# Optimization experiments

Hardware: AMD Instinct MI355X
Metric: run time of the kernel (lower is better)

Reference implementation:

```python
import jax, jax.numpy as jnp
import numpy as np

V = 20000
E = 40000
NODE_IN = 74
EDGE_IN = 12
D = 64            # node_out_feats
EH = 128          # edge_hidden_feats
STEPS = 6         # num_step_message_passing


def setup_inputs() -> dict:
    key = jax.random.key(0)
    ks = jax.random.split(key, 16)
    s = lambda k, shape, scale=0.05: jax.random.normal(k, shape, dtype=jnp.float32) * scale
    return {
        "node_feats": jax.random.normal(ks[0], (V, NODE_IN), dtype=jnp.float32),
        "edge_feats": jax.random.normal(ks[1], (E, EDGE_IN), dtype=jnp.float32),
        "src": jax.random.randint(ks[2], (E,), 0, V),
        "dst": jax.random.randint(ks[3], (E,), 0, V),
        # project_node_feats: Linear(NODE_IN, D) + ReLU
        "proj_W": s(ks[4], (D, NODE_IN)),
        "proj_b": jnp.zeros((D,), jnp.float32),
        # NNConv edge network: Linear(EDGE_IN, EH) -> ReLU -> Linear(EH, D*D)
        "en_W1": s(ks[5], (EH, EDGE_IN)),
        "en_b1": jnp.zeros((EH,), jnp.float32),
        "en_W2": s(ks[6], (D * D, EH)),
        "en_b2": jnp.zeros((D * D,), jnp.float32),
        # NNConv output bias
        "conv_b": jnp.zeros((D,), jnp.float32),
        # single-layer GRU (PyTorch gate order r, z, n)
        "gru_Wih": s(ks[7], (3 * D, D)),
        "gru_Whh": s(ks[8], (3 * D, D)),
        "gru_bih": jnp.zeros((3 * D,), jnp.float32),
        "gru_bhh": jnp.zeros((3 * D,), jnp.float32),
        # MLPPredictor: Linear(2*D, 1)
        "pred_W": s(ks[9], (1, 2 * D)),
        "pred_b": jnp.zeros((1,), jnp.float32),
    }


def reference(node_feats, edge_feats, src, dst, proj_W, proj_b,
              en_W1, en_b1, en_W2, en_b2, conv_b,
              gru_Wih, gru_Whh, gru_bih, gru_bhh, pred_W, pred_b):
    nV = node_feats.shape[0]
    # project node features
    h = jax.nn.relu(node_feats @ proj_W.T + proj_b)  # (V, D)
    # per-edge weight matrices from the edge network (constant across steps)
    ew = jax.nn.relu(edge_feats @ en_W1.T + en_b1) @ en_W2.T + en_b2  # (E, D*D)
    ew = ew.reshape(-1, D, D)  # (E, D, D)

    def step(h, _):
        # NNConv (aggregator='sum'): m_e = h[src_e] @ W_e, sum at dst, + bias
        m = jnp.einsum('ei,eio->eo', h[src], ew)               # (E, D)
        neigh = jax.ops.segment_sum(m, dst, num_segments=nV)   # (V, D)
        x = jax.nn.relu(neigh + conv_b)
        # GRU update; hidden == h (they coincide in the original loop)
        gi = x @ gru_Wih.T + gru_bih
        gh = h @ gru_Whh.T + gru_bhh
        i_r, i_z, i_n = jnp.split(gi, 3, axis=-1)
        h_r, h_z, h_n = jnp.split(gh, 3, axis=-1)
        r = jax.nn.sigmoid(i_r + h_r)
        z = jax.nn.sigmoid(i_z + h_z)
        n = jnp.tanh(i_n + r * h_n)
        h_new = (1.0 - z) * n + z * h
        return h_new, None

    h, _ = jax.lax.scan(step, h, None, length=STEPS)
    # MLPPredictor: per-edge gather-concat-linear
    score = jnp.concatenate([h[src], h[dst]], axis=1) @ pred_W.T + pred_b  # (E, 1)
    return score
```

## Files before the change

kernel.cpp:

```cpp
#include <hip/hip_runtime.h>
#include <hip/hip_bf16.h>
#include <cstdint>

#define NV 20000
#define NE 40000
#define NODE_IN 74
#define EDGE_IN 12
#define D 64
#define EHID 128
#define NSTEPS 6

typedef __bf16 bf16x8 __attribute__((ext_vector_type(8)));
typedef float f32x4 __attribute__((ext_vector_type(4)));

__global__ __launch_bounds__(256) void k_prep(
    const float* __restrict__ nf, const float* __restrict__ pjW, const float* __restrict__ pjb,
    float* __restrict__ h, float* __restrict__ neigh,
    const float* __restrict__ ef, const float* __restrict__ W1, const float* __restrict__ b1,
    __hip_bfloat16* __restrict__ t_bf,
    const float* __restrict__ W2, __hip_bfloat16* __restrict__ w2b,
    const float* __restrict__ b2, __hip_bfloat16* __restrict__ b2t,
    const float* __restrict__ Wih, const float* __restrict__ Whh,
    __hip_bfloat16* __restrict__ Bhi, __hip_bfloat16* __restrict__ Blo) {
  __shared__ float smem[4 * NODE_IN];
  int tid = threadIdx.x;
  int bx = blockIdx.x;
  if (bx < 5000) {
    int nb = bx * 4;
    for (int idx = tid; idx < 4 * NODE_IN; idx += 256)
      smem[idx] = nf[(size_t)nb * NODE_IN + idx];
    __syncthreads();
    int nl = tid >> 6, o = tid & 63;
    float acc = pjb[o];
#pragma unroll
    for (int i = 0; i < NODE_IN; ++i) acc = fmaf(smem[nl * NODE_IN + i], pjW[o * NODE_IN + i], acc);
    h[(size_t)(nb + nl) * D + o] = fmaxf(acc, 0.f);
    neigh[(size_t)(nb + nl) * D + o] = 0.f;
  } else if (bx < 25000) {
    int eb = (bx - 5000) * 2;
    if (tid < 2 * EDGE_IN)
      smem[tid] = ef[(size_t)eb * EDGE_IN + tid];
    __syncthreads();
    int el = tid >> 7, k = tid & 127;
    float acc = b1[k];
#pragma unroll
    for (int j = 0; j < EDGE_IN; ++j) acc = fmaf(smem[el * EDGE_IN + j], W1[k * EDGE_IN + j], acc);
    t_bf[(size_t)(eb + el) * EHID + k] = __float2bfloat16(fmaxf(acc, 0.f));
  } else if (bx < 27048) {
    int idx = (bx - 25000) * 256 + tid;
    w2b[idx] = __float2bfloat16(W2[idx]);
  } else if (bx < 27064) {
    int idx = (bx - 27048) * 256 + tid;
    int o = idx >> 6, i = idx & 63;
    b2t[o * 64 + i] = __float2bfloat16(b2[i * 64 + o]);
  } else {
    int idx = (bx - 27064) * 256 + tid;
    int n = idx >> 7, k = idx & 127;
    int o = n & 63, cls = n >> 6;
    float v;
    if (cls == 0)      v = (k < 64) ? Wih[o * 64 + k]         : Whh[o * 64 + (k - 64)];
    else if (cls == 1) v = (k < 64) ? Wih[(64 + o) * 64 + k]  : Whh[(64 + o) * 64 + (k - 64)];
    else if (cls == 2) v = (k < 64) ? Wih[(128 + o) * 64 + k] : 0.f;
    else               v = (k < 64) ? 0.f                     : Whh[(128 + o) * 64 + (k - 64)];
    __hip_bfloat16 hi = __float2bfloat16(v);
    Bhi[idx] = hi;
    Blo[idx] = __float2bfloat16(v - __bfloat162float(hi));
  }
}

__global__ __launch_bounds__(768, 3) void k_msg(const float* __restrict__ h,
                                                const __hip_bfloat16* __restrict__ t_bf,
                                                const __hip_bfloat16* __restrict__ w2,
                                                const __hip_bfloat16* __restrict__ b2t,
                                                const int* __restrict__ src,
                                                const int* __restrict__ dst,
                                                float* __restrict__ neigh) {
  __shared__ __hip_bfloat16 W2s[512 * 128];
  __shared__ __hip_bfloat16 Hs[12][16 * 64];
  int tid = threadIdx.x;
  int bx = blockIdx.x;
  int cg = bx >> 6, ih = (bx >> 5) & 1, s = bx & 31;
  int lane = tid & 63, lr = lane & 15, lq = lane >> 4;
  int wave = tid >> 6;
  const int ocol = cg * 16 + lr;

  for (int chunk = tid; chunk < 8192; chunk += 768) {
    int row = chunk >> 4, c = chunk & 15;
    int ig = row >> 4, ol = row & 15;
    const __hip_bfloat16* gp =
        w2 + ((size_t)((ih * 32 + ig) * 64 + cg * 16 + ol)) * EHID + c * 8;
    *(bf16x8*)(W2s + row * 128 + ((c ^ ol) * 8)) = *(const bf16x8*)gp;
  }
  bf16x8 b2f0, b2f1;
#pragma unroll
  for (int j = 0; j < 8; ++j) {
    int k = lq * 8 + j;
    __bf16 v = *(const __bf16*)(b2t + (size_t)ocol * 64 + ih * 32 + k);
    __bf16 z = (__bf16)0.0f;
    b2f0[j] = (k < 16) ? v : z;
    b2f1[j] = (k >= 16) ? v : z;
  }
  __syncthreads();

  __hip_bfloat16* Hsw = &Hs[wave][0];
  int e0s = s * 1280;
  int nt = (s < 31) ? 20 : 5;

  int sw0 = (((0 * 4 + lq) ^ lr) * 8);
  int sw1 = (((1 * 4 + lq) ^ lr) * 8);
  int sw2 = (((2 * 4 + lq) ^ lr) * 8);
  int sw3 = (((3 * 4 + lq) ^ lr) * 8);

  int se0 = (wave < nt) ? src[e0s + wave * 64 + lane] : 0;
  int se1 = (wave + 12 < nt) ? src[e0s + (wave + 12) * 64 + lane] : 0;

#pragma unroll 1
  for (int r2 = 0; r2 < 2; ++r2) {
    int t = r2 * 12 + wave;
    if (t >= nt) break;
    int e0t = e0s + t * 64;
    int s_e = r2 ? se1 : se0;

    bf16x8 tf[4][4];
#pragma unroll
    for (int mt = 0; mt < 4; ++mt)
#pragma unroll
      for (int ks = 0; ks < 4; ++ks)
        tf[mt][ks] = *(const bf16x8*)(t_bf + (size_t)(e0t + mt * 16 + lr) * EHID +
                                      ks * 32 + lq * 8);

    int4 dv[4];
#pragma unroll
    for (int mt = 0; mt < 4; ++mt)
      dv[mt] = *(const int4*)(dst + e0t + mt * 16 + lq * 4);

    const float* hrow = h + (size_t)s_e * D + ih * 32;
    f32x4 C[4];
#pragma unroll
    for (int mt = 0; mt < 4; ++mt) C[mt] = f32x4{0.f, 0.f, 0.f, 0.f};

#pragma unroll
    for (int ph = 0; ph < 2; ++ph) {
#pragma unroll
      for (int q = 0; q < 4; ++q) {
        float4 hv = *(const float4*)(hrow + ph * 16 + q * 4);
        Hsw[(q * 4 + 0) * 64 + lane] = __float2bfloat16(hv.x);
        Hsw[(q * 4 + 1) * 64 + lane] = __float2bfloat16(hv.y);
        Hsw[(q * 4 + 2) * 64 + lane] = __float2bfloat16(hv.z);
        Hsw[(q * 4 + 3) * 64 + lane] = __float2bfloat16(hv.w);
      }
#pragma unroll
      for (int mt = 0; mt < 4; ++mt) {
        bf16x8 af;
#pragma unroll
        for (int j = 0; j < 8; ++j)
          af[j] = *(const __bf16*)(Hsw + ((lq * 8 + j) & 15) * 64 + mt * 16 + lr);
        C[mt] = __builtin_amdgcn_mfma_f32_16x16x32_bf16(af, ph ? b2f1 : b2f0, C[mt], 0, 0, 0);
      }
      __builtin_amdgcn_s_setprio(1);
#pragma unroll 2
      for (int igl = 0; igl < 16; ++igl) {
        int ig = ph * 16 + igl;
        const __hip_bfloat16* Wr = W2s + (ig * 16 + lr) * 128;
        bf16x8 f0 = *(const bf16x8*)(Wr + sw0);
        bf16x8 f1 = *(const bf16x8*)(Wr + sw1);
        bf16x8 f2 = *(const bf16x8*)(Wr + sw2);
        bf16x8 f3 = *(const bf16x8*)(Wr + sw3);
#pragma unroll
        for (int mt = 0; mt < 4; ++mt) {
          f32x4 P = {0.f, 0.f, 0.f, 0.f};
          P = __builtin_amdgcn_mfma_f32_16x16x32_bf16(tf[mt][0], f0, P, 0, 0, 0);
          P = __builtin_amdgcn_mfma_f32_16x16x32_bf16(tf[mt][1], f1, P, 0, 0, 0);
          P = __builtin_amdgcn_mfma_f32_16x16x32_bf16(tf[mt][2], f2, P, 0, 0, 0);
          P = __builtin_amdgcn_mfma_f32_16x16x32_bf16(tf[mt][3], f3, P, 0, 0, 0);
          uint2 hA = *(const uint2*)(Hsw + igl * 64 + mt * 16 + lq * 4);
          C[mt][0] = fmaf(__uint_as_float(hA.x << 16), P[0], C[mt][0]);
          C[mt][1] = fmaf(__uint_as_float(hA.x & 0xffff0000u), P[1], C[mt][1]);
          C[mt][2] = fmaf(__uint_as_float(hA.y << 16), P[2], C[mt][2]);
          C[mt][3] = fmaf(__uint_as_float(hA.y & 0xffff0000u), P[3], C[mt][3]);
        }
      }
      __builtin_amdgcn_s_setprio(0);
    }
#pragma unroll
    for (int mt = 0; mt < 4; ++mt) {
      atomicAdd(neigh + (size_t)dv[mt].x * D + ocol, C[mt][0]);
      atomicAdd(neigh + (size_t)dv[mt].y * D + ocol, C[mt][1]);
      atomicAdd(neigh + (size_t)dv[mt].z * D + ocol, C[mt][2]);
      atomicAdd(neigh + (size_t)dv[mt].w * D + ocol, C[mt][3]);
    }
  }
}

__global__ __launch_bounds__(256) void k_gru(float* __restrict__ neigh,
                                             float* __restrict__ h,
                                             const __hip_bfloat16* __restrict__ Bhi,
                                             const __hip_bfloat16* __restrict__ Blo,
                                             const float* __restrict__ cb,
                                             const float* __restrict__ bih,
                                             const float* __restrict__ bhh) {
  __shared__ __hip_bfloat16 Ahi[32 * 128];
  __shared__ __hip_bfloat16 Alo[32 * 128];
  int tid = threadIdx.x;
  int n0 = blockIdx.x * 32;
  for (int idx = tid; idx < 32 * 64; idx += 256) {
    int node = idx >> 6, f = idx & 63;
    int gn = n0 + node;
    float xv = fmaxf(neigh[(size_t)gn * D + f] + cb[f], 0.f);
    neigh[(size_t)gn * D + f] = 0.f;
    float hv = h[(size_t)gn * D + f];
    __hip_bfloat16 xh = __float2bfloat16(xv);
    __hip_bfloat16 hh = __float2bfloat16(hv);
    Ahi[node * 128 + f] = xh;
    Ahi[node * 128 + 64 + f] = hh;
    Alo[node * 128 + f] = __float2bfloat16(xv - __bfloat162float(xh));
    Alo[node * 128 + 64 + f] = __float2bfloat16(hv - __bfloat162float(hh));
  }
  __syncthreads();
  int wave = tid >> 6, lane = tid & 63;
  int lr = lane & 15, lq = lane >> 4;
  f32x4 acc[2][4] = {};
#pragma unroll
  for (int ks = 0; ks < 4; ++ks) {
    int koff = ks * 32 + lq * 8;
    bf16x8 ah[2], al[2], bh[4], bl[4];
#pragma unroll
    for (int mt = 0; mt < 2; ++mt) {
      ah[mt] = *(const bf16x8*)(Ahi + (mt * 16 + lr) * 128 + koff);
      al[mt] = *(const bf16x8*)(Alo + (mt * 16 + lr) * 128 + koff);
    }
#pragma unroll
    for (int cls = 0; cls < 4; ++cls) {
      int n = cls * 64 + wave * 16 + lr;
      bh[cls] = *(const bf16x8*)(Bhi + (size_t)n * 128 + koff);
      bl[cls] = *(const bf16x8*)(Blo + (size_t)n * 128 + koff);
    }
#pragma unroll
    for (int mt = 0; mt < 2; ++mt)
#pragma unroll
      for (int cls = 0; cls < 4; ++cls) {
        acc[mt][cls] = __builtin_amdgcn_mfma_f32_16x16x32_bf16(ah[mt], bh[cls], acc[mt][cls], 0, 0, 0);
        acc[mt][cls] = __builtin_amdgcn_mfma_f32_16x16x32_bf16(al[mt], bh[cls], acc[mt][cls], 0, 0, 0);
        acc[mt][cls] = __builtin_amdgcn_mfma_f32_16x16x32_bf16(ah[mt], bl[cls], acc[mt][cls], 0, 0, 0);
      }
  }
  int o = wave * 16 + lr;
  float b_r = bih[o] + bhh[o];
  float b_z = bih[64 + o] + bhh[64 + o];
  float b_in = bih[128 + o];
  float b_hn = bhh[128 + o];
#pragma unroll
  for (int mt = 0; mt < 2; ++mt) {
#pragma unroll
    for (int r = 0; r < 4; ++r) {
      int gn = n0 + mt * 16 + lq * 4 + r;
      float rs = acc[mt][0][r] + b_r;
      float zs = acc[mt][1][r] + b_z;
      float inn = acc[mt][2][r] + b_in;
      float hnn = acc[mt][3][r] + b_hn;
      float rg = 1.f / (1.f + __expf(-rs));
      float zg = 1.f / (1.f + __expf(-zs));
      float a = inn + rg * hnn;
      a = fminf(fmaxf(a, -15.f), 15.f);
      float e2 = __expf(2.f * a);
      float nn = (e2 - 1.f) / (e2 + 1.f);
      float hold = h[(size_t)gn * D + o];
      h[(size_t)gn * D + o] = (1.f - zg) * nn + zg * hold;
    }
  }
}

__global__ __launch_bounds__(256) void k_pred(const float* __restrict__ h,
                                              const int* __restrict__ src,
                                              const int* __restrict__ dst,
                                              const float* __restrict__ pW,
                                              const float* __restrict__ pb,
                                              float* __restrict__ out) {
  int wave = threadIdx.x >> 6, lane = threadIdx.x & 63;
  int e = blockIdx.x * 4 + wave;
  int s = src[e], d2 = dst[e];
  float v = h[(size_t)s * D + lane] * pW[lane] + h[(size_t)d2 * D + lane] * pW[64 + lane];
#pragma unroll
  for (int off = 32; off >= 1; off >>= 1) v += __shfl_xor(v, off, 64);
  if (lane == 0) out[e] = v + pb[0];
}

extern "C" void kernel_launch(void* const* d_in, const int* in_sizes, int n_in,
                              void* d_out, int out_size, void* d_ws, size_t ws_size,
                              hipStream_t stream) {
  const float* node_feats = (const float*)d_in[0];
  const float* edge_feats = (const float*)d_in[1];
  const int* src = (const int*)d_in[2];
  const int* dst = (const int*)d_in[3];
  const float* proj_W = (const float*)d_in[4];
  const float* proj_b = (const float*)d_in[5];
  const float* en_W1 = (const float*)d_in[6];
  const float* en_b1 = (const float*)d_in[7];
  const float* en_W2 = (const float*)d_in[8];
  const float* en_b2 = (const float*)d_in[9];
  const float* conv_b = (const float*)d_in[10];
  const float* gru_Wih = (const float*)d_in[11];
  const float* gru_Whh = (const float*)d_in[12];
  const float* gru_bih = (const float*)d_in[13];
  const float* gru_bhh = (const float*)d_in[14];
  const float* pred_W = (const float*)d_in[15];
  const float* pred_b = (const float*)d_in[16];

  char* ws = (char*)d_ws;
  size_t off = 0;
  auto walloc = [&](size_t bytes) -> void* {
    void* p = ws + off;
    off = (off + bytes + 255) & ~(size_t)255;
    return p;
  };
  float* h = (float*)walloc((size_t)NV * D * 4);
  float* neigh = (float*)walloc((size_t)NV * D * 4);
  __hip_bfloat16* t_bf = (__hip_bfloat16*)walloc((size_t)NE * EHID * 2);
  __hip_bfloat16* w2_bf = (__hip_bfloat16*)walloc((size_t)D * D * EHID * 2);
  __hip_bfloat16* b2t = (__hip_bfloat16*)walloc((size_t)D * D * 2);
  __hip_bfloat16* Bhi = (__hip_bfloat16*)walloc((size_t)256 * 128 * 2);
  __hip_bfloat16* Blo = (__hip_bfloat16*)walloc((size_t)256 * 128 * 2);

  k_prep<<<27192, 256, 0, stream>>>(node_feats, proj_W, proj_b, h, neigh,
                                    edge_feats, en_W1, en_b1, t_bf,
                                    en_W2, w2_bf, en_b2, b2t,
                                    gru_Wih, gru_Whh, Bhi, Blo);
  for (int s = 0; s < NSTEPS; ++s) {
    k_msg<<<256, 768, 0, stream>>>(h, t_bf, w2_bf, b2t, src, dst, neigh);
    k_gru<<<NV / 32, 256, 0, stream>>>(neigh, h, Bhi, Blo, conv_b, gru_bih, gru_bhh);
  }
  k_pred<<<NE / 4, 256, 0, stream>>>(h, src, dst, pred_W, pred_b, (float*)d_out);
}
```

Before: 519.3 us.

## Shrink k_msg blocks to 512 threads and precompute per-node predictor dot products

k_msg drops from 12 to 8 waves per block, each wave now handling up to three edge tiles. Src and dst indices are loaded inside the loop instead of being prefetched, which lowers register pressure but puts scalar dst loads on the atomic path. The final predictor is split algebraically: the last GRU launch computes per-node dot products with both halves of pred_W, so k_pred only gathers two scalars per edge instead of two 64-float rows. This removes most of the predictor's gather traffic, but the fewer waves per block may reduce latency hiding in the dominant message kernel.

```diff
diff --git a/kernel.cpp b/kernel.cpp
--- a/kernel.cpp
+++ b/kernel.cpp
@@ -68,7 +68,7 @@
   }
 }
 
-__global__ __launch_bounds__(768, 3) void k_msg(const float* __restrict__ h,
+__global__ __launch_bounds__(512, 2) void k_msg(const float* __restrict__ h,
                                                 const __hip_bfloat16* __restrict__ t_bf,
                                                 const __hip_bfloat16* __restrict__ w2,
                                                 const __hip_bfloat16* __restrict__ b2t,
@@ -76,7 +76,7 @@
                                                 const int* __restrict__ dst,
                                                 float* __restrict__ neigh) {
   __shared__ __hip_bfloat16 W2s[512 * 128];
-  __shared__ __hip_bfloat16 Hs[12][16 * 64];
+  __shared__ __hip_bfloat16 Hs[8][16 * 64];
   int tid = threadIdx.x;
   int bx = blockIdx.x;
   int cg = bx >> 6, ih = (bx >> 5) & 1, s = bx & 31;
@@ -84,7 +84,9 @@
   int wave = tid >> 6;
   const int ocol = cg * 16 + lr;
 
-  for (int chunk = tid; chunk < 8192; chunk += 768) {
+#pragma unroll
+  for (int it = 0; it < 16; ++it) {
+    int chunk = it * 512 + tid;
     int row = chunk >> 4, c = chunk & 15;
     int ig = row >> 4, ol = row & 15;
     const __hip_bfloat16* gp =
@@ -111,15 +113,11 @@
   int sw2 = (((2 * 4 + lq) ^ lr) * 8);
   int sw3 = (((3 * 4 + lq) ^ lr) * 8);
 
-  int se0 = (wave < nt) ? src[e0s + wave * 64 + lane] : 0;
-  int se1 = (wave + 12 < nt) ? src[e0s + (wave + 12) * 64 + lane] : 0;
-
 #pragma unroll 1
-  for (int r2 = 0; r2 < 2; ++r2) {
-    int t = r2 * 12 + wave;
+  for (int r3 = 0; r3 < 3; ++r3) {
+    int t = r3 * 8 + wave;
     if (t >= nt) break;
     int e0t = e0s + t * 64;
-    int s_e = r2 ? se1 : se0;
 
     bf16x8 tf[4][4];
 #pragma unroll
@@ -129,11 +127,7 @@
         tf[mt][ks] = *(const bf16x8*)(t_bf + (size_t)(e0t + mt * 16 + lr) * EHID +
                                       ks * 32 + lq * 8);
 
-    int4 dv[4];
-#pragma unroll
-    for (int mt = 0; mt < 4; ++mt)
-      dv[mt] = *(const int4*)(dst + e0t + mt * 16 + lq * 4);
-
+    int s_e = src[e0t + lane];
     const float* hrow = h + (size_t)s_e * D + ih * 32;
     f32x4 C[4];
 #pragma unroll
@@ -184,10 +178,11 @@
     }
 #pragma unroll
     for (int mt = 0; mt < 4; ++mt) {
-      atomicAdd(neigh + (size_t)dv[mt].x * D + ocol, C[mt][0]);
-      atomicAdd(neigh + (size_t)dv[mt].y * D + ocol, C[mt][1]);
-      atomicAdd(neigh + (size_t)dv[mt].z * D + ocol, C[mt][2]);
-      atomicAdd(neigh + (size_t)dv[mt].w * D + ocol, C[mt][3]);
+#pragma unroll
+      for (int r = 0; r < 4; ++r) {
+        int ea = e0t + mt * 16 + lq * 4 + r;
+        atomicAdd(neigh + (size_t)dst[ea] * D + ocol, C[mt][r]);
+      }
     }
   }
 }
@@ -198,7 +193,11 @@
                                              const __hip_bfloat16* __restrict__ Blo,
                                              const float* __restrict__ cb,
                                              const float* __restrict__ bih,
-                                             const float* __restrict__ bhh) {
+                                             const float* __restrict__ bhh,
+                                             const float* __restrict__ pW,
+                                             float* __restrict__ pa,
+                                             float* __restrict__ pbv,
+                                             int last) {
   __shared__ __hip_bfloat16 Ahi[32 * 128];
   __shared__ __hip_bfloat16 Alo[32 * 128];
   int tid = threadIdx.x;
@@ -268,21 +267,34 @@
       h[(size_t)gn * D + o] = (1.f - zg) * nn + zg * hold;
     }
   }
-}
-
-__global__ __launch_bounds__(256) void k_pred(const float* __restrict__ h,
+  if (last) {
+    __syncthreads();
+    int node = tid >> 3, o0 = (tid & 7) * 8;
+    int gn = n0 + node;
+    float sa = 0.f, sb = 0.f;
+#pragma unroll
+    for (int j = 0; j < 8; ++j) {
+      float hv = h[(size_t)gn * D + o0 + j];
+      sa = fmaf(hv, pW[o0 + j], sa);
+      sb = fmaf(hv, pW[64 + o0 + j], sb);
+    }
+#pragma unroll
+    for (int off = 4; off >= 1; off >>= 1) {
+      sa += __shfl_xor(sa, off, 64);
+      sb += __shfl_xor(sb, off, 64);
+    }
+    if ((tid & 7) == 0) { pa[gn] = sa; pbv[gn] = sb; }
+  }
+}
+
+__global__ __launch_bounds__(256) void k_pred(const float* __restrict__ pa,
+                                              const float* __restrict__ pbv,
                                               const int* __restrict__ src,
                                               const int* __restrict__ dst,
-                                              const float* __restrict__ pW,
                                               const float* __restrict__ pb,
                                               float* __restrict__ out) {
-  int wave = threadIdx.x >> 6, lane = threadIdx.x & 63;
-  int e = blockIdx.x * 4 + wave;
-  int s = src[e], d2 = dst[e];
-  float v = h[(size_t)s * D + lane] * pW[lane] + h[(size_t)d2 * D + lane] * pW[64 + lane];
-#pragma unroll
-  for (int off = 32; off >= 1; off >>= 1) v += __shfl_xor(v, off, 64);
-  if (lane == 0) out[e] = v + pb[0];
+  int e = blockIdx.x * 256 + threadIdx.x;
+  if (e < NE) out[e] = pa[src[e]] + pbv[dst[e]] + pb[0];
 }
 
 extern "C" void kernel_launch(void* const* d_in, const int* in_sizes, int n_in,
@@ -320,14 +332,17 @@
   __hip_bfloat16* b2t = (__hip_bfloat16*)walloc((size_t)D * D * 2);
   __hip_bfloat16* Bhi = (__hip_bfloat16*)walloc((size_t)256 * 128 * 2);
   __hip_bfloat16* Blo = (__hip_bfloat16*)walloc((size_t)256 * 128 * 2);
+  float* pa = (float*)walloc((size_t)NV * 4);
+  float* pbv = (float*)walloc((size_t)NV * 4);
 
   k_prep<<<27192, 256, 0, stream>>>(node_feats, proj_W, proj_b, h, neigh,
                                     edge_feats, en_W1, en_b1, t_bf,
                                     en_W2, w2_bf, en_b2, b2t,
                                     gru_Wih, gru_Whh, Bhi, Blo);
   for (int s = 0; s < NSTEPS; ++s) {
-    k_msg<<<256, 768, 0, stream>>>(h, t_bf, w2_bf, b2t, src, dst, neigh);
-    k_gru<<<NV / 32, 256, 0, stream>>>(neigh, h, Bhi, Blo, conv_b, gru_bih, gru_bhh);
-  }
-  k_pred<<<NE / 4, 256, 0, stream>>>(h, src, dst, pred_W, pred_b, (float*)d_out);
-}
+    k_msg<<<256, 512, 0, stream>>>(h, t_bf, w2_bf, b2t, src, dst, neigh);
+    k_gru<<<NV / 32, 256, 0, stream>>>(neigh, h, Bhi, Blo, conv_b, gru_bih, gru_bhh,
+                                       pred_W, pa, pbv, (s == NSTEPS - 1) ? 1 : 0);
+  }
+  k_pred<<<(NE + 255) / 256, 256, 0, stream>>>(pa, pbv, src, dst, pred_b, (float*)d_out);
+}
```

Measured after the change: 488.2 us. -6.0%, faster.
